# Optimization experiments

Hardware: AMD Instinct MI355X
Metric: run time of the kernel (lower is better)

The kernel has to match this reference:

```python
import jax, jax.numpy as jnp
import numpy as np

B, C, H, W = 8, 64, 256, 256


def _conv1x1(x, w, b):
    # x: [B,Cin,H,W], w: [Cout,Cin], b: [Cout]
    return jnp.einsum('bchw,oc->bohw', x, w) + b[None, :, None, None]


def setup_inputs() -> dict:
    key = jax.random.key(0)
    ks = jax.random.split(key, 6)
    return {
        'hs': jax.random.normal(ks[0], (B, C, H, W), jnp.float32),
        'ref_LR': jax.random.normal(ks[1], (B, 9, H, W), jnp.float32),
        'w_first': jax.random.normal(ks[2], (C, 9), jnp.float32) * 0.1,
        'b_first': jax.random.normal(ks[3], (C,), jnp.float32) * 0.1,
        'w_fuse': jax.random.normal(ks[4], (C, 2 * C), jnp.float32) * 0.05,
        'b_fuse': jax.random.normal(ks[5], (C,), jnp.float32) * 0.1,
    }


def reference(hs, ref_LR, w_first, b_first, w_fuse, b_fuse):
    # 1x1 conv + LeakyReLU(0.1) on the 9-channel reference
    ref = jax.nn.leaky_relu(_conv1x1(ref_LR, w_first, b_first), 0.1)  # [B,C,H,W]
    pad = ((0, 0), (0, 0), (1, 1), (1, 1))
    # Per-pixel, per-channel 3x3 windowed dot product of hs-patch and ref-patch
    # == 3x3 box-sum of the elementwise product (both reflect-padded).
    p = jnp.pad(hs, pad, mode='reflect') * jnp.pad(ref, pad, mode='reflect')
    h, w = hs.shape[2], hs.shape[3]
    cross = jnp.zeros_like(hs)
    for dy in range(3):  # fixed 3x3 window, not a data-dim loop
        for dx in range(3):
            cross = cross + p[:, :, dy:dy + h, dx:dx + w]
    att = jax.nn.sigmoid(cross)            # [B,C,H,W]
    fused = jnp.concatenate((att * hs, hs), axis=1)  # [B,2C,H,W]
    return _conv1x1(fused, w_fuse, b_fuse)  # [B,C,H,W]
```

## Files before the change

### kernel.cpp

```cpp
#include <hip/hip_runtime.h>

#define BB 8
#define CC 64
#define HH 256
#define WW 256
#define HW (HH*WW)

typedef __attribute__((ext_vector_type(8))) short bf16x8;
typedef __attribute__((ext_vector_type(4))) float f32x4;
typedef __attribute__((ext_vector_type(2))) float f32x2;

__device__ __forceinline__ int reflect_idx(int v, int n) {
    if (v < 0) v = -v;
    if (v >= n) v = 2*n - 2 - v;
    return v;
}

__device__ __forceinline__ short f2bf(float f) {
    union { float f; unsigned u; } x; x.f = f;
    unsigned r = (x.u + 0x7fffu + ((x.u >> 16) & 1u)) >> 16;
    return (short)r;
}

__device__ __forceinline__ unsigned cvt_pk_bf16(float lo, float hi) {
    unsigned r;
    asm("v_cvt_pk_bf16_f32 %0, %1, %2" : "=v"(r) : "v"(lo), "v"(hi));
    return r;
}

__global__ __launch_bounds__(256, 3)
void corr_wave_kernel(const float* __restrict__ hs,
                      const float* __restrict__ refLR,
                      const float* __restrict__ w_first,
                      const float* __restrict__ b_first,
                      const float* __restrict__ w_fuse,
                      const float* __restrict__ b_fuse,
                      float* __restrict__ out) {
    __shared__ short s_w[64 * 136];
    __shared__ short s_fused[4][64 * 40];
    __shared__ float s_p01[4][200];
    __shared__ float s_p23[4][200];

    const int t = threadIdx.x;
    const int wv = t >> 6, lane = t & 63;

    const int d = (int)blockIdx.x;
    const int lid = (d & 7) * 256 + (d >> 3);
    const int bx = lid & 15, by = (lid >> 4) & 15, b = lid >> 8;

    #pragma unroll
    for (int r = 0; r < 32; ++r) {
        int idx = t + r * 256;
        int m = idx >> 7, kp = idx & 127;
        int g = kp >> 5, i = kp & 31;
        int src = (i < 16) ? (g * 16 + i) : (48 + g * 16 + i);
        s_w[m * 136 + kp] = f2bf(w_fuse[m * 128 + src]);
    }
    __syncthreads();

    const int wy = (wv >> 1) * 8, wx = (wv & 1) * 8;
    const int y0 = by * 16 + wy, x0 = bx * 16 + wx;

    const bool has1 = lane < 36;
    int g0, g1;
    {
        const int py = lane / 10, px = lane % 10;
        g0 = reflect_idx(y0 + py - 1, HH) * WW + reflect_idx(x0 + px - 1, WW);
    }
    {
        const int pp = 64 + lane;
        const int py = pp / 10, px = pp % 10;
        g1 = has1 ? (reflect_idx(y0 + py - 1, HH) * WW + reflect_idx(x0 + px - 1, WW)) : g0;
    }
    const int pyc = lane >> 3, pxc = lane & 7;
    const int gc = (y0 + pyc) * WW + (x0 + pxc);

    const float* rb = refLR + (size_t)b * 9 * HW;
    float rin0[9], rin1[9];
    #pragma unroll
    for (int j = 0; j < 9; ++j) rin0[j] = rb[(size_t)j * HW + g0];
    #pragma unroll
    for (int j = 0; j < 9; ++j) rin1[j] = rb[(size_t)j * HW + g1];

    const int cl = lane & 15, kb = lane >> 4;
    f32x4 acc[4][4];
    #pragma unroll
    for (int mt = 0; mt < 4; ++mt) {
        #pragma unroll
        for (int r = 0; r < 4; ++r) {
            const float bv = b_fuse[mt * 16 + kb * 4 + r];
            #pragma unroll
            for (int nt = 0; nt < 4; ++nt) acc[mt][nt][r] = bv;
        }
    }

    const float* hsb = hs + (size_t)b * CC * HW;
    float* const sp01 = s_p01[wv];
    float* const sp23 = s_p23[wv];
    short* const sfw  = s_fused[wv];
    const int pb = (pyc * 10 + pxc) * 2;

    float h0[4], h1[4], hc[4];
    #pragma unroll
    for (int cc = 0; cc < 4; ++cc) {
        const float* hp = hsb + (size_t)cc * HW;
        h0[cc] = hp[g0]; h1[cc] = hp[g1]; hc[cc] = hp[gc];
    }

    #pragma unroll 1
    for (int ch = 0; ch < 16; ++ch) {
        const int c0 = ch * 4;

        float pr0[4], pr1[4], hcv[4];
        #pragma unroll
        for (int cc = 0; cc < 4; ++cc) {
            const int c = c0 + cc;
            float v0 = b_first[c], v1 = v0;
            #pragma unroll
            for (int j = 0; j < 9; ++j) {
                const float w = w_first[c * 9 + j];
                v0 = fmaf(w, rin0[j], v0);
                v1 = fmaf(w, rin1[j], v1);
            }
            v0 = v0 > 0.f ? v0 : 0.1f * v0;
            v1 = v1 > 0.f ? v1 : 0.1f * v1;
            pr0[cc] = h0[cc] * v0;
            pr1[cc] = h1[cc] * v1;
            hcv[cc] = hc[cc];
        }
        *(f32x2*)&sp01[lane * 2] = (f32x2){pr0[0], pr0[1]};
        *(f32x2*)&sp23[lane * 2] = (f32x2){pr0[2], pr0[3]};
        if (has1) {
            *(f32x2*)&sp01[(64 + lane) * 2] = (f32x2){pr1[0], pr1[1]};
            *(f32x2*)&sp23[(64 + lane) * 2] = (f32x2){pr1[2], pr1[3]};
        }
        asm volatile("s_waitcnt lgkmcnt(0)" ::: "memory");

        f32x2 a01 = (f32x2){0.f, 0.f}, a23 = (f32x2){0.f, 0.f};
        #pragma unroll
        for (int dy = 0; dy < 3; ++dy)
            #pragma unroll
            for (int dx = 0; dx < 3; ++dx) {
                const int o = pb + (dy * 10 + dx) * 2;
                a01 += *(const f32x2*)&sp01[o];
                a23 += *(const f32x2*)&sp23[o];
            }

        {
            const int cn = ((ch + 1) & 15) * 4;
            #pragma unroll
            for (int cc = 0; cc < 4; ++cc) {
                const float* hp = hsb + (size_t)(cn + cc) * HW;
                h0[cc] = hp[g0]; h1[cc] = hp[g1]; hc[cc] = hp[gc];
            }
        }

        const float cr[4] = {a01[0], a01[1], a23[0], a23[1]};
        float av[4];
        #pragma unroll
        for (int cc = 0; cc < 4; ++cc)
            av[cc] = __builtin_amdgcn_rcpf(
                1.0f + __builtin_amdgcn_exp2f(cr[cc] * -1.44269504088896f)) * hcv[cc];
        uint2 ua, uh;
        ua.x = cvt_pk_bf16(av[0], av[1]);
        ua.y = cvt_pk_bf16(av[2], av[3]);
        uh.x = cvt_pk_bf16(hcv[0], hcv[1]);
        uh.y = cvt_pk_bf16(hcv[2], hcv[3]);
        const int k4 = (ch & 3) * 4;
        *(uint2*)&sfw[lane * 40 + k4] = ua;
        *(uint2*)&sfw[lane * 40 + 16 + k4] = uh;

        if ((ch & 3) == 3) {
            asm volatile("s_waitcnt lgkmcnt(0)" ::: "memory");
            const int g = ch >> 2;
            #pragma unroll
            for (int nt = 0; nt < 4; ++nt) {
                const bf16x8 bf = *(const bf16x8*)&sfw[(nt * 16 + cl) * 40 + kb * 8];
                #pragma unroll
                for (int mt = 0; mt < 4; ++mt) {
                    const bf16x8 af = *(const bf16x8*)&s_w[(mt * 16 + cl) * 136 + g * 32 + kb * 8];
                    acc[mt][nt] = __builtin_amdgcn_mfma_f32_16x16x32_bf16(af, bf, acc[mt][nt], 0, 0, 0);
                }
            }
        }
    }

    float* const ob = out + (size_t)b * CC * HW;
    #pragma unroll
    for (int mt = 0; mt < 4; ++mt) {
        const int o0 = mt * 16 + kb * 4;
        #pragma unroll
        for (int nt = 0; nt < 4; ++nt) {
            const int p = nt * 16 + cl;
            float* op = ob + (size_t)o0 * HW + (size_t)(y0 + (p >> 3)) * WW + (x0 + (p & 7));
            #pragma unroll
            for (int r = 0; r < 4; ++r) op[(size_t)r * HW] = acc[mt][nt][r];
        }
    }
}

extern "C" void kernel_launch(void* const* d_in, const int* in_sizes, int n_in,
                              void* d_out, int out_size, void* d_ws, size_t ws_size,
                              hipStream_t stream) {
    const float* hs      = (const float*)d_in[0];
    const float* refLR   = (const float*)d_in[1];
    const float* w_first = (const float*)d_in[2];
    const float* b_first = (const float*)d_in[3];
    const float* w_fuse  = (const float*)d_in[4];
    const float* b_fuse  = (const float*)d_in[5];
    float* out = (float*)d_out;

    corr_wave_kernel<<<dim3(2048), dim3(256), 0, stream>>>(hs, refLR, w_first, b_first,
                                                           w_fuse, b_fuse, out);
}
```

Baseline: 122.2 us.

## Replace LDS row padding with XOR swizzles and raise occupancy target to 4

After: 228.1 us. +86.6%, slower.

```diff
diff --git a/kernel.cpp b/kernel.cpp
--- a/kernel.cpp
+++ b/kernel.cpp
@@ -28,18 +28,19 @@
     return r;
 }
 
-__global__ __launch_bounds__(256, 3)
-void corr_wave_kernel(const float* __restrict__ hs,
-                      const float* __restrict__ refLR,
-                      const float* __restrict__ w_first,
-                      const float* __restrict__ b_first,
-                      const float* __restrict__ w_fuse,
-                      const float* __restrict__ b_fuse,
-                      float* __restrict__ out) {
-    __shared__ short s_w[64 * 136];
-    __shared__ short s_fused[4][64 * 40];
-    __shared__ float s_p01[4][200];
-    __shared__ float s_p23[4][200];
+__global__ __launch_bounds__(256, 4)
+void corr_v7_kernel(const float* __restrict__ hs,
+                    const float* __restrict__ refLR,
+                    const float* __restrict__ w_first,
+                    const float* __restrict__ b_first,
+                    const float* __restrict__ w_fuse,
+                    const float* __restrict__ b_fuse,
+                    float* __restrict__ out)
+{
+    __shared__ short s_w[64 * 128];
+    __shared__ short s_fused[4][64 * 32];
+    __shared__ float s_p01[4][240];
+    __shared__ float s_p23[4][240];
 
     const int t = threadIdx.x;
     const int wv = t >> 6, lane = t & 63;
@@ -49,12 +50,13 @@
     const int bx = lid & 15, by = (lid >> 4) & 15, b = lid >> 8;
 
     #pragma unroll
-    for (int r = 0; r < 32; ++r) {
-        int idx = t + r * 256;
-        int m = idx >> 7, kp = idx & 127;
-        int g = kp >> 5, i = kp & 31;
+    for (int rep = 0; rep < 32; ++rep) {
+        int idx = t + rep * 256;
+        int m = idx >> 7, k = idx & 127;
+        int g = k >> 5, i = k & 31;
         int src = (i < 16) ? (g * 16 + i) : (48 + g * 16 + i);
-        s_w[m * 136 + kp] = f2bf(w_fuse[m * 128 + src]);
+        int swz = ((((k >> 3) ^ m) & 15) << 3) | (k & 7);
+        s_w[m * 128 + swz] = f2bf(w_fuse[m * 128 + src]);
     }
     __syncthreads();
 
@@ -67,11 +69,15 @@
         const int py = lane / 10, px = lane % 10;
         g0 = reflect_idx(y0 + py - 1, HH) * WW + reflect_idx(x0 + px - 1, WW);
     }
+    const int l1 = 64 + lane;
     {
-        const int pp = 64 + lane;
-        const int py = pp / 10, px = pp % 10;
-        g1 = has1 ? (reflect_idx(y0 + py - 1, HH) * WW + reflect_idx(x0 + px - 1, WW)) : g0;
-    }
+        const int py = l1 / 10, px = l1 % 10;
+        const int gt = reflect_idx(y0 + py - 1, HH) * WW + reflect_idx(x0 + px - 1, WW);
+        g1 = has1 ? gt : g0;
+    }
+    const int pos0 = (lane / 10) * 12 + lane % 10;
+    const int pos1 = (l1 / 10) * 12 + l1 % 10;
+
     const int pyc = lane >> 3, pxc = lane & 7;
     const int gc = (y0 + pyc) * WW + (x0 + pxc);
 
@@ -98,7 +104,8 @@
     float* const sp01 = s_p01[wv];
     float* const sp23 = s_p23[wv];
     short* const sfw  = s_fused[wv];
-    const int pb = (pyc * 10 + pxc) * 2;
+    const int pb = (pyc * 12 + pxc) * 2;
+    const int skey = (lane >> 1) & 3;
 
     float h0[4], h1[4], hc[4];
     #pragma unroll
@@ -128,11 +135,11 @@
             pr1[cc] = h1[cc] * v1;
             hcv[cc] = hc[cc];
         }
-        *(f32x2*)&sp01[lane * 2] = (f32x2){pr0[0], pr0[1]};
-        *(f32x2*)&sp23[lane * 2] = (f32x2){pr0[2], pr0[3]};
+        *(f32x2*)&sp01[pos0 * 2] = (f32x2){pr0[0], pr0[1]};
+        *(f32x2*)&sp23[pos0 * 2] = (f32x2){pr0[2], pr0[3]};
         if (has1) {
-            *(f32x2*)&sp01[(64 + lane) * 2] = (f32x2){pr1[0], pr1[1]};
-            *(f32x2*)&sp23[(64 + lane) * 2] = (f32x2){pr1[2], pr1[3]};
+            *(f32x2*)&sp01[pos1 * 2] = (f32x2){pr1[0], pr1[1]};
+            *(f32x2*)&sp23[pos1 * 2] = (f32x2){pr1[2], pr1[3]};
         }
         asm volatile("s_waitcnt lgkmcnt(0)" ::: "memory");
 
@@ -141,7 +148,7 @@
         for (int dy = 0; dy < 3; ++dy)
             #pragma unroll
             for (int dx = 0; dx < 3; ++dx) {
-                const int o = pb + (dy * 10 + dx) * 2;
+                const int o = pb + (dy * 12 + dx) * 2;
                 a01 += *(const f32x2*)&sp01[o];
                 a23 += *(const f32x2*)&sp23[o];
             }
@@ -167,18 +174,23 @@
         uh.x = cvt_pk_bf16(hcv[0], hcv[1]);
         uh.y = cvt_pk_bf16(hcv[2], hcv[3]);
         const int k4 = (ch & 3) * 4;
-        *(uint2*)&sfw[lane * 40 + k4] = ua;
-        *(uint2*)&sfw[lane * 40 + 16 + k4] = uh;
+        const int ga = (ch & 3) >> 1;
+        const int oa = k4 & 7;
+        *(uint2*)&sfw[lane * 32 + ((ga       ^ skey) << 3) + oa] = ua;
+        *(uint2*)&sfw[lane * 32 + (((2 + ga) ^ skey) << 3) + oa] = uh;
 
         if ((ch & 3) == 3) {
             asm volatile("s_waitcnt lgkmcnt(0)" ::: "memory");
             const int g = ch >> 2;
             #pragma unroll
             for (int nt = 0; nt < 4; ++nt) {
-                const bf16x8 bf = *(const bf16x8*)&sfw[(nt * 16 + cl) * 40 + kb * 8];
+                const int p = nt * 16 + cl;
+                const bf16x8 bf = *(const bf16x8*)
+                    &sfw[p * 32 + ((kb ^ ((p >> 1) & 3)) << 3)];
                 #pragma unroll
                 for (int mt = 0; mt < 4; ++mt) {
-                    const bf16x8 af = *(const bf16x8*)&s_w[(mt * 16 + cl) * 136 + g * 32 + kb * 8];
+                    const bf16x8 af = *(const bf16x8*)
+                        &s_w[(mt * 16 + cl) * 128 + (((g * 4 + kb) ^ cl) << 3)];
                     acc[mt][nt] = __builtin_amdgcn_mfma_f32_16x16x32_bf16(af, bf, acc[mt][nt], 0, 0, 0);
                 }
             }
@@ -210,6 +222,6 @@
     const float* b_fuse  = (const float*)d_in[5];
     float* out = (float*)d_out;
 
-    corr_wave_kernel<<<dim3(2048), dim3(256), 0, stream>>>(hs, refLR, w_first, b_first,
-                                                           w_fuse, b_fuse, out);
-}
+    corr_v7_kernel<<<dim3(2048), dim3(256), 0, stream>>>(hs, refLR, w_first, b_first,
+                                                         w_fuse, b_fuse, out);
+}
```
